# Optimization experiments

Measured on AMD Instinct MI355X. Metric: run time of the kernel, lower is better.

## Reference

```python
import jax, jax.numpy as jnp
import numpy as np

B, N, K, C = 8, 4096, 16, 64
OUT = [128, 128, 128]
BN_EPS = 1e-3


def setup_inputs() -> dict:
    key = jax.random.key(0)
    ks = jax.random.split(key, 8)
    inp = {
        "points1": jax.random.normal(ks[0], (B, 3, N), jnp.float32),
        "points2": jax.random.normal(ks[1], (B, 3, N), jnp.float32),
        "features1": jax.random.normal(ks[2], (B, C, N), jnp.float32),
        "features2": jax.random.normal(ks[3], (B, C, N), jnp.float32),
    }
    dims = [2 * C + 3] + OUT  # [131, 128, 128, 128]
    for i in range(len(OUT)):
        kw = jax.random.fold_in(ks[4], i)
        inp[f"W{i}"] = jax.random.normal(kw, (dims[i + 1], dims[i]), jnp.float32) / np.sqrt(dims[i]).astype(np.float32)
        inp[f"b{i}"] = jnp.zeros((dims[i + 1],), jnp.float32)
        inp[f"gamma{i}"] = jnp.ones((dims[i + 1],), jnp.float32)
        inp[f"beta{i}"] = jnp.zeros((dims[i + 1],), jnp.float32)
    return inp


def _knn_group(points2, points1, features2):
    # points*: [B, 3, N].  For each query in points1, find K nearest in points2.
    d = jnp.sum((points1[:, :, :, None] - points2[:, :, None, :]) ** 2, axis=1)  # [B, Nq, Ns]
    _, idx = jax.lax.top_k(-d, K)  # [B, Nq, K]
    idx_b = idx[:, None, :, :]  # [B, 1, Nq, K] broadcasts over channel dim
    xyz_g = jnp.take_along_axis(points2[:, :, None, :], idx_b, axis=3)      # [B, 3, Nq, K]
    rel_xyz = xyz_g - points1[:, :, :, None]                                # relative coords
    feat_g = jnp.take_along_axis(features2[:, :, None, :], idx_b, axis=3)  # [B, C, Nq, K]
    return jnp.concatenate([rel_xyz, feat_g], axis=1)  # [B, C+3, Nq, K]


def _conv_bn_relu(x, W, b, gamma, beta):
    # 1x1 conv == per-position channel matmul; BN in training mode (batch stats, biased var)
    x = jnp.einsum('oc,bcnk->bonk', W, x) + b[None, :, None, None]
    mu = jnp.mean(x, axis=(0, 2, 3), keepdims=True)
    var = jnp.var(x, axis=(0, 2, 3), keepdims=True)
    x = (x - mu) * jax.lax.rsqrt(var + BN_EPS)
    x = x * gamma[None, :, None, None] + beta[None, :, None, None]
    return jax.nn.relu(x)


def reference(points1, points2, features1, features2,
              W0, b0, gamma0, beta0,
              W1, b1, gamma1, beta1,
              W2, b2, gamma2, beta2):
    g = _knn_group(points2, points1, features2)                       # [B, C+3, N, K]
    f1 = jnp.broadcast_to(features1[:, :, :, None], (B, C, N, K))     # expand over neighbors
    x = jnp.concatenate([g, f1], axis=1)                              # [B, 2C+3, N, K]
    x = _conv_bn_relu(x, W0, b0, gamma0, beta0)
    x = _conv_bn_relu(x, W1, b1, gamma1, beta1)
    x = _conv_bn_relu(x, W2, b2, gamma2, beta2)
    return jnp.max(x, axis=3)                                         # [B, OUT[-1], N]
```

## Files before the change

kernel.cpp:

```cpp
#include <hip/hip_runtime.h>
#include <hip/hip_bf16.h>

#define B_ 8
#define N_ 4096
#define K_ 16
#define C_ 64
#define NK_ (N_*K_)
#define M_ (B_*N_*K_)
#define BN_EPS_ 0.001f
#define CH_ 16
#define CS_ (N_/CH_)
#define Q_ (B_*N_)
#define NB1_ (M_/128)

typedef short bf16x8 __attribute__((ext_vector_type(8)));
typedef float f32x4 __attribute__((ext_vector_type(4)));

static __device__ __forceinline__ unsigned pk2bf(float a, float b) {
  union { __hip_bfloat162 h; unsigned u; } c;
  c.h = __float22bfloat162_rn(make_float2(a, b));
  return c.u;
}
static __device__ __forceinline__ unsigned short f2bf1(float x) {
  union { __hip_bfloat16 h; unsigned short u; } c;
  c.h = __float2bfloat16(x);
  return c.u;
}

__global__ __launch_bounds__(256) void pack_pts(const float* __restrict__ p,
                                                float4* __restrict__ pf4) {
  int i = blockIdx.x * 256 + threadIdx.x;
  int b = i >> 12;
  int n = i & (N_ - 1);
  const float* base = p + (size_t)b * 3 * N_;
  pf4[i] = make_float4(base[n], base[N_ + n], base[2 * N_ + n], 0.f);
}

__global__ __launch_bounds__(256) void wcvt(const float* __restrict__ W,
                                            unsigned short* __restrict__ Wb) {
  int i = blockIdx.x * 256 + threadIdx.x;
  Wb[i] = f2bf1(W[i]);
}

__global__ void make_w0at(const float* __restrict__ W0, float* __restrict__ w0at) {
  int o = threadIdx.x;
  for (int d = 0; d < 3; ++d) w0at[d * 128 + o] = W0[o * 131 + d];
}

__global__ void zero_stats(float* __restrict__ stats) {
  int i = blockIdx.x * 256 + threadIdx.x;
  stats[i] = 0.f;
}

__global__ __launch_bounds__(64) void knn_part(const float4* __restrict__ p1f4,
                                               const float4* __restrict__ p2f4,
                                               float* __restrict__ pvals) {
  int lane = threadIdx.x;
  int blk = blockIdx.x;
  int chunk = blk & (CH_ - 1);
  int grp = (blk >> 4) & 63;
  int b = blk >> 10;
  int n1 = (grp << 6) + lane;
  int q = (b << 12) + n1;
  float4 qv = p1f4[q];
  float ax = qv.x, ay = qv.y, az = qv.z;
  const float4* pb = p2f4 + ((size_t)b << 12) + chunk * CS_;

  float s[16];
  #pragma unroll
  for (int i = 0; i < 16; ++i) s[i] = 3.0e38f;

  #pragma unroll 8
  for (int t = 0; t < CS_; ++t) {
    float4 c = pb[t];
    float dx = ax - c.x, dy = ay - c.y, dz = az - c.z;
    float d = __fadd_rn(__fadd_rn(__fmul_rn(dx, dx), __fmul_rn(dy, dy)), __fmul_rn(dz, dz));
    #pragma unroll
    for (int i = 0; i < 15; ++i) s[i] = __builtin_amdgcn_fmed3f(s[i], s[i + 1], d);
    s[15] = fminf(s[15], d);
  }
  #pragma unroll
  for (int i = 0; i < 16; ++i) pvals[(size_t)(chunk * 16 + i) * Q_ + q] = s[i];
}

__global__ __launch_bounds__(256) void knn_merge(const float* __restrict__ pvals,
                                                 float* __restrict__ Tarr) {
  int q = blockIdx.x * 256 + threadIdx.x;
  float s[16];
  #pragma unroll
  for (int i = 0; i < 16; ++i) s[i] = 3.0e38f;
  #pragma unroll 8
  for (int t = 0; t < CH_ * 16; ++t) {
    float d = pvals[(size_t)t * Q_ + q];
    #pragma unroll
    for (int i = 0; i < 15; ++i) s[i] = __builtin_amdgcn_fmed3f(s[i], s[i + 1], d);
    s[15] = fminf(s[15], d);
  }
  Tarr[q] = s[0];
}

__global__ __launch_bounds__(64) void knn_cand(const float4* __restrict__ p1f4,
                                               const float4* __restrict__ p2f4,
                                               const float* __restrict__ Tarr,
                                               int* __restrict__ cidx,
                                               int* __restrict__ ccnt) {
  int lane = threadIdx.x;
  int blk = blockIdx.x;
  int chunk = blk & (CH_ - 1);
  int grp = (blk >> 4) & 63;
  int b = blk >> 10;
  int n1 = (grp << 6) + lane;
  int q = (b << 12) + n1;
  float4 qq = p1f4[q];
  float ax = qq.x, ay = qq.y, az = qq.z;
  const float4* pb = p2f4 + ((size_t)b << 12) + chunk * CS_;
  float T = Tarr[q];
  int cnt = 0;
  int base = (q * CH_ + chunk) * 16;
  #pragma unroll 4
  for (int t = 0; t < CS_; ++t) {
    float4 c = pb[t];
    float dx = ax - c.x, dy = ay - c.y, dz = az - c.z;
    float d = __fadd_rn(__fadd_rn(__fmul_rn(dx, dx), __fmul_rn(dy, dy)), __fmul_rn(dz, dz));
    if (d <= T && cnt < 16) { cidx[base + cnt] = chunk * CS_ + t; ++cnt; }
  }
  ccnt[q * CH_ + chunk] = cnt;
}

__global__ __launch_bounds__(256) void knn_combine(const int* __restrict__ cidx,
                                                   const int* __restrict__ ccnt,
                                                   int* __restrict__ idxout) {
  int q = blockIdx.x * 256 + threadIdx.x;
  int tot = 0;
  int ob = q * 16;
  for (int c = 0; c < CH_; ++c) {
    int m = ccnt[q * CH_ + c];
    const int* src = cidx + (size_t)(q * CH_ + c) * 16;
    for (int i = 0; i < m && tot < 16; ++i) idxout[ob + tot++] = src[i];
  }
}

__global__ __launch_bounds__(256) void pkern(const float* __restrict__ f,
                                             const float* __restrict__ W0,
                                             const float* __restrict__ bias,
                                             const float4* __restrict__ pf4,
                                             const float* __restrict__ w0at,
                                             float sgn,
                                             float* __restrict__ P, int coff) {
  __shared__ float fx[32 * 65];
  __shared__ __align__(16) float Wl[64 * 132];
  int tid = threadIdx.x;
  int bn0 = blockIdx.x * 32;
  int b = bn0 >> 12, nb0 = bn0 & (N_ - 1);

  for (int u = tid; u < 32 * 64; u += 256) {
    int c = u >> 5, nl = u & 31;
    fx[nl * 65 + c] = f[((size_t)b * C_ + c) * N_ + nb0 + nl];
  }
  for (int u = tid; u < 128 * 64; u += 256) {
    int o = u >> 6, c = u & 63;
    Wl[c * 132 + o] = W0[o * 131 + coff + c];
  }
  __syncthreads();

  int og = tid & 15, np_ = tid >> 4;
  int o0 = og * 8;
  int na = np_ * 2, nb = na + 1;
  float acc0[8], acc1[8];
  #pragma unroll
  for (int j = 0; j < 8; ++j) {
    float bv = bias ? bias[o0 + j] : 0.f;
    acc0[j] = bv; acc1[j] = bv;
  }
  for (int c = 0; c < 64; ++c) {
    float x0 = fx[na * 65 + c], x1 = fx[nb * 65 + c];
    float4 wa = *(const float4*)&Wl[c * 132 + o0];
    float4 wb = *(const float4*)&Wl[c * 132 + o0 + 4];
    float w[8] = {wa.x, wa.y, wa.z, wa.w, wb.x, wb.y, wb.z, wb.w};
    #pragma unroll
    for (int j = 0; j < 8; ++j) {
      acc0[j] = fmaf(x0, w[j], acc0[j]);
      acc1[j] = fmaf(x1, w[j], acc1[j]);
    }
  }
  float4 pa = pf4[bn0 + na], pb_ = pf4[bn0 + nb];
  #pragma unroll
  for (int j = 0; j < 8; ++j) {
    float wx = w0at[o0 + j], wy = w0at[128 + o0 + j], wz = w0at[256 + o0 + j];
    acc0[j] += sgn * (wx * pa.x + wy * pa.y + wz * pa.z);
    acc1[j] += sgn * (wx * pb_.x + wy * pb_.y + wz * pb_.z);
  }
  float* Pa = P + (size_t)(bn0 + na) * 128 + o0;
  float* Pb = P + (size_t)(bn0 + nb) * 128 + o0;
  *(float4*)Pa = make_float4(acc0[0], acc0[1], acc0[2], acc0[3]);
  *(float4*)(Pa + 4) = make_float4(acc0[4], acc0[5], acc0[6], acc0[7]);
  *(float4*)Pb = make_float4(acc1[0], acc1[1], acc1[2], acc1[3]);
  *(float4*)(Pb + 4) = make_float4(acc1[4], acc1[5], acc1[6], acc1[7]);
}

__global__ __launch_bounds__(256) void gstats_kernel(
    const float* __restrict__ A, const float* __restrict__ Bv,
    const int* __restrict__ idx, unsigned short* __restrict__ x0b,
    float* __restrict__ part) {
  __shared__ float sred[4 * 128 * 2];
  int tid = threadIdx.x;
  int R0 = blockIdx.x * 128;
  int b = R0 >> 16;
  int n0 = (R0 & (NK_ - 1)) >> 4;
  int cc = (tid & 15) * 8;
  int r0l = tid >> 4;

  int jj[8];
  #pragma unroll
  for (int p = 0; p < 8; ++p) jj[p] = idx[R0 + r0l + p * 16];

  float ssum[8], ssq[8];
  #pragma unroll
  for (int u = 0; u < 8; ++u) { ssum[u] = 0.f; ssq[u] = 0.f; }

  #pragma unroll
  for (int p = 0; p < 8; ++p) {
    const float* Ar = A + (size_t)((b << 12) + n0 + p) * 128 + cc;
    const float* Br = Bv + (size_t)((b << 12) + jj[p]) * 128 + cc;
    float av[8], bv[8];
    *(float4*)&av[0] = *(const float4*)Ar;  *(float4*)&av[4] = *(const float4*)(Ar + 4);
    *(float4*)&bv[0] = *(const float4*)Br;  *(float4*)&bv[4] = *(const float4*)(Br + 4);
    unsigned pw[4];
    #pragma unroll
    for (int i = 0; i < 4; ++i)
      pw[i] = pk2bf(av[2 * i] + bv[2 * i], av[2 * i + 1] + bv[2 * i + 1]);
    uint4 pk; pk.x = pw[0]; pk.y = pw[1]; pk.z = pw[2]; pk.w = pw[3];
    *(uint4*)(x0b + (size_t)(R0 + r0l + p * 16) * 128 + cc) = pk;
    #pragma unroll
    for (int i = 0; i < 4; ++i) {
      float q0 = __uint_as_float(pw[i] << 16);
      float q1 = __uint_as_float(pw[i] & 0xFFFF0000u);
      ssum[2 * i] += q0;     ssq[2 * i] = fmaf(q0, q0, ssq[2 * i]);
      ssum[2 * i + 1] += q1; ssq[2 * i + 1] = fmaf(q1, q1, ssq[2 * i + 1]);
    }
  }
  int w = tid >> 6, lane = tid & 63;
  #pragma unroll
  for (int u = 0; u < 8; ++u) {
    ssum[u] += __shfl_xor(ssum[u], 16);
    ssum[u] += __shfl_xor(ssum[u], 32);
    ssq[u] += __shfl_xor(ssq[u], 16);
    ssq[u] += __shfl_xor(ssq[u], 32);
  }
  if (lane < 16) {
    #pragma unroll
    for (int u = 0; u < 8; ++u) {
      sred[(w * 128 + lane * 8 + u) * 2] = ssum[u];
      sred[(w * 128 + lane * 8 + u) * 2 + 1] = ssq[u];
    }
  }
  __syncthreads();
  if (tid < 128) {
    float a = 0.f, q2 = 0.f;
    #pragma unroll
    for (int ww = 0; ww < 4; ++ww) {
      a += sred[(ww * 128 + tid) * 2];
      q2 += sred[(ww * 128 + tid) * 2 + 1];
    }
    part[(size_t)blockIdx.x * 256 + tid] = a;
    part[(size_t)blockIdx.x * 256 + 128 + tid] = q2;
  }
}

__global__ __launch_bounds__(256) void reduce_atomic(const float* __restrict__ part,
                                                     float* __restrict__ statso) {
  int tid = threadIdx.x;
  int r0 = blockIdx.x * 16;
  float a = 0.f;
  #pragma unroll
  for (int i = 0; i < 16; ++i) a += part[(size_t)(r0 + i) * 256 + tid];
  atomicAdd(statso + tid, a);
}

__global__ void bnfin_kernel(const float* __restrict__ stats, const float* __restrict__ gamma,
                             const float* __restrict__ beta, float* __restrict__ bnp) {
  int o = threadIdx.x;
  const float invM = 1.0f / (float)M_;
  float mean = stats[o] * invM;
  float var = stats[128 + o] * invM - mean * mean;
  float s = gamma[o] * rsqrtf(var + BN_EPS_);
  bnp[o] = s;
  bnp[128 + o] = beta[o] - mean * s;
}

static __device__ __forceinline__ char* xsa(unsigned short* Xs, int row, int bytecol) {
  return (char*)Xs + row * 256 + (bytecol ^ ((row & 7) << 4));
}

static __device__ __forceinline__ void stage_lin(
    unsigned short* Xs, const unsigned short* x0b, const float* bnp0,
    int R0, int tid) {
  int cc = (tid & 15) * 8;
  int r0l = tid >> 4;
  float svv[8], tvv[8];
  *(float4*)&svv[0] = *(const float4*)(bnp0 + cc);       *(float4*)&svv[4] = *(const float4*)(bnp0 + cc + 4);
  *(float4*)&tvv[0] = *(const float4*)(bnp0 + 128 + cc); *(float4*)&tvv[4] = *(const float4*)(bnp0 + 132 + cc);
  #pragma unroll
  for (int p = 0; p < 8; ++p) {
    uint4 pv = *(const uint4*)(x0b + (size_t)(R0 + r0l + p * 16) * 128 + cc);
    float xv[8];
    xv[0] = __uint_as_float(pv.x << 16); xv[1] = __uint_as_float(pv.x & 0xFFFF0000u);
    xv[2] = __uint_as_float(pv.y << 16); xv[3] = __uint_as_float(pv.y & 0xFFFF0000u);
    xv[4] = __uint_as_float(pv.z << 16); xv[5] = __uint_as_float(pv.z & 0xFFFF0000u);
    xv[6] = __uint_as_float(pv.w << 16); xv[7] = __uint_as_float(pv.w & 0xFFFF0000u);
    float y[8];
    #pragma unroll
    for (int u = 0; u < 8; ++u) y[u] = fmaxf(fmaf(svv[u], xv[u], tvv[u]), 0.f);
    uint4 pk;
    pk.x = pk2bf(y[0], y[1]); pk.y = pk2bf(y[2], y[3]);
    pk.z = pk2bf(y[4], y[5]); pk.w = pk2bf(y[6], y[7]);
    *(uint4*)xsa(Xs, r0l + p * 16, 16 * (tid & 15)) = pk;
  }
}

__global__ __launch_bounds__(256) void pass1_kernel(
    const unsigned short* __restrict__ x0b, const float* __restrict__ bnp0,
    const unsigned short* __restrict__ W1b, const float* __restrict__ b1,
    float* __restrict__ part) {
  __shared__ __align__(16) unsigned short Xs[128 * 128];
  int tid = threadIdx.x;
  int R0 = blockIdx.x * 128;

  stage_lin(Xs, x0b, bnp0, R0, tid);

  int w = tid >> 6, lane = tid & 63;
  int m16 = lane & 15, qd = lane >> 4;

  bf16x8 bf[2][4];
  #pragma unroll
  for (int nt = 0; nt < 2; ++nt) {
    const unsigned short* wb = W1b + (size_t)(w * 32 + nt * 16 + m16) * 128 + qd * 8;
    #pragma unroll
    for (int q = 0; q < 4; ++q) bf[nt][q] = *(const bf16x8*)(wb + q * 32);
  }
  __syncthreads();

  f32x4 acc[8][2];
  #pragma unroll
  for (int m = 0; m < 8; ++m) {
    acc[m][0] = (f32x4){0.f, 0.f, 0.f, 0.f};
    acc[m][1] = (f32x4){0.f, 0.f, 0.f, 0.f};
  }
  #pragma unroll
  for (int m = 0; m < 8; ++m) {
    bf16x8 a[4];
    #pragma unroll
    for (int q = 0; q < 4; ++q) a[q] = *(const bf16x8*)xsa(Xs, m * 16 + m16, 16 * qd + 64 * q);
    #pragma unroll
    for (int q = 0; q < 4; ++q) {
      acc[m][0] = __builtin_amdgcn_mfma_f32_16x16x32_bf16(a[q], bf[0][q], acc[m][0], 0, 0, 0);
      acc[m][1] = __builtin_amdgcn_mfma_f32_16x16x32_bf16(a[q], bf[1][q], acc[m][1], 0, 0, 0);
    }
  }

  float ssum[2] = {0.f, 0.f}, ssq[2] = {0.f, 0.f};
  #pragma unroll
  for (int nt = 0; nt < 2; ++nt) {
    float bb = b1[w * 32 + nt * 16 + m16];
    #pragma unroll
    for (int m = 0; m < 8; ++m)
      #pragma unroll
      for (int rg = 0; rg < 4; ++rg) {
        float y = acc[m][nt][rg] + bb;
        ssum[nt] += y;
        ssq[nt] = fmaf(y, y, ssq[nt]);
      }
  }
  #pragma unroll
  for (int nt = 0; nt < 2; ++nt) {
    ssum[nt] += __shfl_xor(ssum[nt], 16);
    ssum[nt] += __shfl_xor(ssum[nt], 32);
    ssq[nt] += __shfl_xor(ssq[nt], 16);
    ssq[nt] += __shfl_xor(ssq[nt], 32);
  }
  if (lane < 16) {
    size_t pb = (size_t)blockIdx.x * 256 + w * 32;
    #pragma unroll
    for (int nt = 0; nt < 2; ++nt) {
      part[pb + nt * 16 + lane] = ssum[nt];
      part[pb + 128 + nt * 16 + lane] = ssq[nt];
    }
  }
}

__global__ __launch_bounds__(256) void pass2_kernel(
    const unsigned short* __restrict__ x0b, const float* __restrict__ bnp0,
    const unsigned short* __restrict__ W1b, const float* __restrict__ b1,
    const float* __restrict__ bnp1, const unsigned short* __restrict__ W2b,
    const float* __restrict__ b2, float* __restrict__ ymaxo,
    float* __restrict__ ymino, float* __restrict__ part) {
  __shared__ __align__(16) unsigned short Xs[128 * 128];
  int tid = threadIdx.x;
  int R0 = blockIdx.x * 128;
  int b = R0 >> 16;
  int n0 = (R0 & (NK_ - 1)) >> 4;

  stage_lin(Xs, x0b, bnp0, R0, tid);

  int w = tid >> 6, lane = tid & 63;
  int m16 = lane & 15, qd = lane >> 4;

  bf16x8 bf[2][4];
  #pragma unroll
  for (int nt = 0; nt < 2; ++nt) {
    const unsigned short* wb = W1b + (size_t)(w * 32 + nt * 16 + m16) * 128 + qd * 8;
    #pragma unroll
    for (int q = 0; q < 4; ++q) bf[nt][q] = *(const bf16x8*)(wb + q * 32);
  }
  __syncthreads();

  f32x4 acc[8][2];
  #pragma unroll
  for (int m = 0; m < 8; ++m) {
    acc[m][0] = (f32x4){0.f, 0.f, 0.f, 0.f};
    acc[m][1] = (f32x4){0.f, 0.f, 0.f, 0.f};
  }
  #pragma unroll
  for (int m = 0; m < 8; ++m) {
    bf16x8 a[4];
    #pragma unroll
    for (int q = 0; q < 4; ++q) a[q] = *(const bf16x8*)xsa(Xs, m * 16 + m16, 16 * qd + 64 * q);
    #pragma unroll
    for (int q = 0; q < 4; ++q) {
      acc[m][0] = __builtin_amdgcn_mfma_f32_16x16x32_bf16(a[q], bf[0][q], acc[m][0], 0, 0, 0);
      acc[m][1] = __builtin_amdgcn_mfma_f32_16x16x32_bf16(a[q], bf[1][q], acc[m][1], 0, 0, 0);
    }
  }
  __syncthreads();

  #pragma unroll
  for (int nt = 0; nt < 2; ++nt) {
    int col = w * 32 + nt * 16 + m16;
    float sc = bnp1[col];
    float tc = fmaf(sc, b1[col], bnp1[128 + col]);
    #pragma unroll
    for (int m = 0; m < 8; ++m)
      #pragma unroll
      for (int rg = 0; rg < 4; ++rg) {
        int row = m * 16 + qd * 4 + rg;
        float y = fmaxf(fmaf(sc, acc[m][nt][rg], tc), 0.f);
        *(unsigned short*)xsa(Xs, row, 2 * col) = f2bf1(y);
      }
  }

  bf16x8 bf2[2][4];
  #pragma unroll
  for (int nt = 0; nt < 2; ++nt) {
    const unsigned short* wb = W2b + (size_t)(w * 32 + nt * 16 + m16) * 128 + qd * 8;
    #pragma unroll
    for (int q = 0; q < 4; ++q) bf2[nt][q] = *(const bf16x8*)(wb + q * 32);
  }
  __syncthreads();

  #pragma unroll
  for (int m = 0; m < 8; ++m) {
    acc[m][0] = (f32x4){0.f, 0.f, 0.f, 0.f};
    acc[m][1] = (f32x4){0.f, 0.f, 0.f, 0.f};
  }
  #pragma unroll
  for (int m = 0; m < 8; ++m) {
    bf16x8 a[4];
    #pragma unroll
    for (int q = 0; q < 4; ++q) a[q] = *(const bf16x8*)xsa(Xs, m * 16 + m16, 16 * qd + 64 * q);
    #pragma unroll
    for (int q = 0; q < 4; ++q) {
      acc[m][0] = __builtin_amdgcn_mfma_f32_16x16x32_bf16(a[q], bf2[0][q], acc[m][0], 0, 0, 0);
      acc[m][1] = __builtin_amdgcn_mfma_f32_16x16x32_bf16(a[q], bf2[1][q], acc[m][1], 0, 0, 0);
    }
  }

  float ssum[2] = {0.f, 0.f}, ssq[2] = {0.f, 0.f};
  #pragma unroll
  for (int nt = 0; nt < 2; ++nt) {
    float bb = b2[w * 32 + nt * 16 + m16];
    #pragma unroll
    for (int m = 0; m < 8; ++m) {
      float y0 = acc[m][nt][0] + bb;
      float mx = y0, mn = y0, su = y0, sq = y0 * y0;
      #pragma unroll
      for (int rg = 1; rg < 4; ++rg) {
        float y = acc[m][nt][rg] + bb;
        mx = fmaxf(mx, y); mn = fminf(mn, y);
        su += y; sq = fmaf(y, y, sq);
      }
      mx = fmaxf(mx, __shfl_xor(mx, 16)); mx = fmaxf(mx, __shfl_xor(mx, 32));
      mn = fminf(mn, __shfl_xor(mn, 16)); mn = fminf(mn, __shfl_xor(mn, 32));
      ssum[nt] += su; ssq[nt] += sq;
      if (lane < 16) {
        int n = n0 + m;
        size_t basey = ((size_t)(b << 12) + n) * 128 + w * 32 + nt * 16 + lane;
        ymaxo[basey] = mx;
        ymino[basey] = mn;
      }
    }
  }
  #pragma unroll
  for (int nt = 0; nt < 2; ++nt) {
    ssum[nt] += __shfl_xor(ssum[nt], 16);
    ssum[nt] += __shfl_xor(ssum[nt], 32);
    ssq[nt] += __shfl_xor(ssq[nt], 16);
    ssq[nt] += __shfl_xor(ssq[nt], 32);
  }
  if (lane < 16) {
    size_t pb = (size_t)blockIdx.x * 256 + w * 32;
    #pragma unroll
    for (int nt = 0; nt < 2; ++nt) {
      part[pb + nt * 16 + lane] = ssum[nt];
      part[pb + 128 + nt * 16 + lane] = ssq[nt];
    }
  }
}

__global__ __launch_bounds__(256) void final_kernel(const float* __restrict__ ymaxo,
                                                    const float* __restrict__ ymino,
                                                    const float* __restrict__ bnp2,
                                                    float* __restrict__ out) {
  __shared__ float T[64 * 129];
  int tid = threadIdx.x;
  int b = blockIdx.x >> 6;
  int n0 = (blockIdx.x & 63) * 64;
  for (int u = tid; u < 64 * 128; u += 256) {
    int nl = u >> 7, o = u & 127;
    size_t base = ((size_t)(b << 12) + n0 + nl) * 128 + o;
    float s = bnp2[o], t = bnp2[128 + o];
    float v = fmaf(s, (s >= 0.f ? ymaxo[base] : ymino[base]), t);
    T[nl * 129 + o] = fmaxf(v, 0.f);
  }
  __syncthreads();
  for (int u = tid; u < 64 * 128; u += 256) {
    int o = u >> 6, nl = u & 63;
    out[((size_t)b * 128 + o) * N_ + n0 + nl] = T[nl * 129 + o];
  }
}

extern "C" void kernel_launch(void* const* d_in, const int* in_sizes, int n_in,
                              void* d_out, int out_size, void* d_ws, size_t ws_size,
                              hipStream_t stream) {
  (void)in_sizes; (void)n_in; (void)out_size; (void)ws_size;
  const float* points1 = (const float*)d_in[0];
  const float* points2 = (const float*)d_in[1];
  const float* features1 = (const float*)d_in[2];
  const float* features2 = (const float*)d_in[3];
  const float* W0 = (const float*)d_in[4];
  const float* b0 = (const float*)d_in[5];
  const float* g0 = (const float*)d_in[6];
  const float* be0 = (const float*)d_in[7];
  const float* W1 = (const float*)d_in[8];
  const float* b1 = (const float*)d_in[9];
  const float* g1 = (const float*)d_in[10];
  const float* be1 = (const float*)d_in[11];
  const float* W2 = (const float*)d_in[12];
  const float* b2 = (const float*)d_in[13];
  const float* g2 = (const float*)d_in[14];
  const float* be2 = (const float*)d_in[15];
  float* out = (float*)d_out;

  char* ws = (char*)d_ws;
  size_t off = 0;
  auto alloc = [&](size_t bytes) -> void* {
    void* p = ws + off;
    off += (bytes + 255) & ~(size_t)255;
    return p;
  };
  int* idx = (int*)alloc((size_t)M_ * 4);
  float4* p1f4 = (float4*)alloc((size_t)B_ * N_ * 16);
  float4* p2f4 = (float4*)alloc((size_t)B_ * N_ * 16);
  float* A = (float*)alloc((size_t)B_ * N_ * 128 * 4);
  float* Bv = (float*)alloc((size_t)B_ * N_ * 128 * 4);
  unsigned short* W1b = (unsigned short*)alloc(128 * 128 * 2);
  unsigned short* W2b = (unsigned short*)alloc(128 * 128 * 2);
  float* w0at = (float*)alloc(3 * 128 * 4);
  float* stats = (float*)alloc(3 * 256 * 4);
  float* bnp = (float*)alloc(3 * 256 * 4);
  float* ymaxo = (float*)alloc((size_t)B_ * N_ * 128 * 4);
  float* ymino = (float*)alloc((size_t)B_ * N_ * 128 * 4);
  char* bigbuf = (char*)alloc((size_t)128 * 1024 * 1024);
  float* pvals = (float*)bigbuf;
  int* cidx = (int*)(bigbuf + (size_t)32 * 1024 * 1024);
  int* ccnt = (int*)(bigbuf + (size_t)64 * 1024 * 1024);
  float* Tarr = (float*)(bigbuf + (size_t)66 * 1024 * 1024);
  unsigned short* x0b = (unsigned short*)bigbuf;

  float* part0 = ymaxo;
  float* part1 = ymino;
  float* part2 = A;

  zero_stats<<<3, 256, 0, stream>>>(stats);
  pack_pts<<<B_ * N_ / 256, 256, 0, stream>>>(points1, p1f4);
  pack_pts<<<B_ * N_ / 256, 256, 0, stream>>>(points2, p2f4);
  wcvt<<<64, 256, 0, stream>>>(W1, W1b);
  wcvt<<<64, 256, 0, stream>>>(W2, W2b);
  make_w0at<<<1, 128, 0, stream>>>(W0, w0at);

  knn_part<<<B_ * 64 * CH_, 64, 0, stream>>>(p1f4, p2f4, pvals);
  knn_merge<<<Q_ / 256, 256, 0, stream>>>(pvals, Tarr);
  knn_cand<<<B_ * 64 * CH_, 64, 0, stream>>>(p1f4, p2f4, Tarr, cidx, ccnt);
  knn_combine<<<Q_ / 256, 256, 0, stream>>>(cidx, ccnt, idx);

  pkern<<<B_ * N_ / 32, 256, 0, stream>>>(features1, W0, b0, p1f4, w0at, -1.f, A, 67);
  pkern<<<B_ * N_ / 32, 256, 0, stream>>>(features2, W0, nullptr, p2f4, w0at, 1.f, Bv, 3);

  gstats_kernel<<<NB1_, 256, 0, stream>>>(A, Bv, idx, x0b, part0);
  reduce_atomic<<<NB1_ / 16, 256, 0, stream>>>(part0, stats);
  bnfin_kernel<<<1, 128, 0, stream>>>(stats, g0, be0, bnp);

  pass1_kernel<<<NB1_, 256, 0, stream>>>(x0b, bnp, W1b, b1, part1);
  reduce_atomic<<<NB1_ / 16, 256, 0, stream>>>(part1, stats + 256);
  bnfin_kernel<<<1, 128, 0, stream>>>(stats + 256, g1, be1, bnp + 256);

  pass2_kernel<<<NB1_, 256, 0, stream>>>(x0b, bnp, W1b, b1, bnp + 256,
                                         W2b, b2, ymaxo, ymino, part2);
  reduce_atomic<<<NB1_ / 16, 256, 0, stream>>>(part2, stats + 512);
  bnfin_kernel<<<1, 128, 0, stream>>>(stats + 512, g2, be2, bnp + 512);

  final_kernel<<<B_ * N_ / 64, 256, 0, stream>>>(ymaxo, ymino, bnp + 512, out);
}
```

Baseline: 495.3 us.

## Derive KNN threshold from a point subset, then filter and select candidates

New measurement: 624.7 us. 26.1% more time.

```diff
diff --git a/kernel.cpp b/kernel.cpp
--- a/kernel.cpp
+++ b/kernel.cpp
@@ -8,10 +8,9 @@
 #define NK_ (N_*K_)
 #define M_ (B_*N_*K_)
 #define BN_EPS_ 0.001f
-#define CH_ 16
-#define CS_ (N_/CH_)
 #define Q_ (B_*N_)
 #define NB1_ (M_/128)
+#define CAP_ 48
 
 typedef short bf16x8 __attribute__((ext_vector_type(8)));
 typedef float f32x4 __attribute__((ext_vector_type(4)));
@@ -25,6 +24,11 @@
   union { __hip_bfloat16 h; unsigned short u; } c;
   c.h = __float2bfloat16(x);
   return c.u;
+}
+
+static __device__ __forceinline__ float knn_key(float ax, float ay, float az, float4 c) {
+  float dx = ax - c.x, dy = ay - c.y, dz = az - c.z;
+  return __fadd_rn(__fadd_rn(__fmul_rn(dx, dx), __fmul_rn(dy, dy)), __fmul_rn(dz, dz));
 }
 
 __global__ __launch_bounds__(256) void pack_pts(const float* __restrict__ p,
@@ -52,45 +56,42 @@
   stats[i] = 0.f;
 }
 
-__global__ __launch_bounds__(64) void knn_part(const float4* __restrict__ p1f4,
-                                               const float4* __restrict__ p2f4,
-                                               float* __restrict__ pvals) {
+__global__ __launch_bounds__(64) void knn_sub(const float4* __restrict__ p1f4,
+                                              const float4* __restrict__ p2f4,
+                                              float* __restrict__ pvals) {
   int lane = threadIdx.x;
   int blk = blockIdx.x;
-  int chunk = blk & (CH_ - 1);
-  int grp = (blk >> 4) & 63;
-  int b = blk >> 10;
-  int n1 = (grp << 6) + lane;
-  int q = (b << 12) + n1;
+  int c = blk & 3;
+  int grp = (blk >> 2) & 63;
+  int b = blk >> 8;
+  int q = (b << 12) + (grp << 6) + lane;
   float4 qv = p1f4[q];
   float ax = qv.x, ay = qv.y, az = qv.z;
-  const float4* pb = p2f4 + ((size_t)b << 12) + chunk * CS_;
+  const float4* pb = p2f4 + ((size_t)b << 12) + c * 128;
 
   float s[16];
   #pragma unroll
   for (int i = 0; i < 16; ++i) s[i] = 3.0e38f;
 
   #pragma unroll 8
-  for (int t = 0; t < CS_; ++t) {
-    float4 c = pb[t];
-    float dx = ax - c.x, dy = ay - c.y, dz = az - c.z;
-    float d = __fadd_rn(__fadd_rn(__fmul_rn(dx, dx), __fmul_rn(dy, dy)), __fmul_rn(dz, dz));
+  for (int t = 0; t < 128; ++t) {
+    float d = knn_key(ax, ay, az, pb[t]);
     #pragma unroll
     for (int i = 0; i < 15; ++i) s[i] = __builtin_amdgcn_fmed3f(s[i], s[i + 1], d);
     s[15] = fminf(s[15], d);
   }
   #pragma unroll
-  for (int i = 0; i < 16; ++i) pvals[(size_t)(chunk * 16 + i) * Q_ + q] = s[i];
-}
-
-__global__ __launch_bounds__(256) void knn_merge(const float* __restrict__ pvals,
-                                                 float* __restrict__ Tarr) {
+  for (int i = 0; i < 16; ++i) pvals[(size_t)(c * 16 + i) * Q_ + q] = s[i];
+}
+
+__global__ __launch_bounds__(256) void knn_t0(const float* __restrict__ pvals,
+                                              float* __restrict__ Tarr) {
   int q = blockIdx.x * 256 + threadIdx.x;
   float s[16];
   #pragma unroll
   for (int i = 0; i < 16; ++i) s[i] = 3.0e38f;
   #pragma unroll 8
-  for (int t = 0; t < CH_ * 16; ++t) {
+  for (int t = 0; t < 64; ++t) {
     float d = pvals[(size_t)t * Q_ + q];
     #pragma unroll
     for (int i = 0; i < 15; ++i) s[i] = __builtin_amdgcn_fmed3f(s[i], s[i + 1], d);
@@ -99,44 +100,61 @@
   Tarr[q] = s[0];
 }
 
-__global__ __launch_bounds__(64) void knn_cand(const float4* __restrict__ p1f4,
-                                               const float4* __restrict__ p2f4,
-                                               const float* __restrict__ Tarr,
-                                               int* __restrict__ cidx,
-                                               int* __restrict__ ccnt) {
+__global__ __launch_bounds__(64) void knn_collect(const float4* __restrict__ p1f4,
+                                                  const float4* __restrict__ p2f4,
+                                                  const float* __restrict__ Tarr,
+                                                  uint2* __restrict__ cbuf,
+                                                  int* __restrict__ ccnt) {
   int lane = threadIdx.x;
   int blk = blockIdx.x;
-  int chunk = blk & (CH_ - 1);
-  int grp = (blk >> 4) & 63;
-  int b = blk >> 10;
-  int n1 = (grp << 6) + lane;
-  int q = (b << 12) + n1;
-  float4 qq = p1f4[q];
-  float ax = qq.x, ay = qq.y, az = qq.z;
-  const float4* pb = p2f4 + ((size_t)b << 12) + chunk * CS_;
+  int c = blk & 7;
+  int grp = (blk >> 3) & 63;
+  int b = blk >> 9;
+  int q = (b << 12) + (grp << 6) + lane;
+  float4 qv = p1f4[q];
+  float ax = qv.x, ay = qv.y, az = qv.z;
+  const float4* pb = p2f4 + ((size_t)b << 12) + c * 512;
   float T = Tarr[q];
   int cnt = 0;
-  int base = (q * CH_ + chunk) * 16;
   #pragma unroll 4
-  for (int t = 0; t < CS_; ++t) {
-    float4 c = pb[t];
-    float dx = ax - c.x, dy = ay - c.y, dz = az - c.z;
-    float d = __fadd_rn(__fadd_rn(__fmul_rn(dx, dx), __fmul_rn(dy, dy)), __fmul_rn(dz, dz));
-    if (d <= T && cnt < 16) { cidx[base + cnt] = chunk * CS_ + t; ++cnt; }
-  }
-  ccnt[q * CH_ + chunk] = cnt;
-}
-
-__global__ __launch_bounds__(256) void knn_combine(const int* __restrict__ cidx,
-                                                   const int* __restrict__ ccnt,
-                                                   int* __restrict__ idxout) {
+  for (int t = 0; t < 512; ++t) {
+    float d = knn_key(ax, ay, az, pb[t]);
+    if (d <= T && cnt < CAP_) {
+      cbuf[(size_t)(c * CAP_ + cnt) * Q_ + q] = make_uint2(__float_as_uint(d), c * 512 + t);
+      ++cnt;
+    }
+  }
+  ccnt[c * Q_ + q] = cnt;
+}
+
+__global__ __launch_bounds__(256) void knn_final(const uint2* __restrict__ cbuf,
+                                                 const int* __restrict__ ccnt,
+                                                 int* __restrict__ idxout) {
   int q = blockIdx.x * 256 + threadIdx.x;
-  int tot = 0;
-  int ob = q * 16;
-  for (int c = 0; c < CH_; ++c) {
-    int m = ccnt[q * CH_ + c];
-    const int* src = cidx + (size_t)(q * CH_ + c) * 16;
-    for (int i = 0; i < m && tot < 16; ++i) idxout[ob + tot++] = src[i];
+  float s[16];
+  #pragma unroll
+  for (int i = 0; i < 16; ++i) s[i] = 3.0e38f;
+  int cn[8];
+  #pragma unroll
+  for (int c = 0; c < 8; ++c) {
+    int m = ccnt[c * Q_ + q];
+    cn[c] = m;
+    for (int i = 0; i < m; ++i) {
+      float d = __uint_as_float(cbuf[(size_t)(c * CAP_ + i) * Q_ + q].x);
+      #pragma unroll
+      for (int k = 0; k < 15; ++k) s[k] = __builtin_amdgcn_fmed3f(s[k], s[k + 1], d);
+      s[15] = fminf(s[15], d);
+    }
+  }
+  float T = s[0];
+  int tot = 0, ob = q * 16;
+  #pragma unroll
+  for (int c = 0; c < 8; ++c) {
+    int m = cn[c];
+    for (int i = 0; i < m && tot < 16; ++i) {
+      uint2 e = cbuf[(size_t)(c * CAP_ + i) * Q_ + q];
+      if (__uint_as_float(e.x) <= T) idxout[ob + tot++] = (int)e.y;
+    }
   }
 }
 
@@ -580,10 +598,10 @@
   float* ymaxo = (float*)alloc((size_t)B_ * N_ * 128 * 4);
   float* ymino = (float*)alloc((size_t)B_ * N_ * 128 * 4);
   char* bigbuf = (char*)alloc((size_t)128 * 1024 * 1024);
-  float* pvals = (float*)bigbuf;
-  int* cidx = (int*)(bigbuf + (size_t)32 * 1024 * 1024);
-  int* ccnt = (int*)(bigbuf + (size_t)64 * 1024 * 1024);
-  float* Tarr = (float*)(bigbuf + (size_t)66 * 1024 * 1024);
+  uint2* cbuf = (uint2*)bigbuf;
+  float* pvals = (float*)(bigbuf + (size_t)98 * 1024 * 1024);
+  float* Tarr = (float*)(bigbuf + (size_t)107 * 1024 * 1024);
+  int* ccnt = (int*)(bigbuf + (size_t)108 * 1024 * 1024);
   unsigned short* x0b = (unsigned short*)bigbuf;
 
   float* part0 = ymaxo;
@@ -597,10 +615,10 @@
   wcvt<<<64, 256, 0, stream>>>(W2, W2b);
   make_w0at<<<1, 128, 0, stream>>>(W0, w0at);
 
-  knn_part<<<B_ * 64 * CH_, 64, 0, stream>>>(p1f4, p2f4, pvals);
-  knn_merge<<<Q_ / 256, 256, 0, stream>>>(pvals, Tarr);
-  knn_cand<<<B_ * 64 * CH_, 64, 0, stream>>>(p1f4, p2f4, Tarr, cidx, ccnt);
-  knn_combine<<<Q_ / 256, 256, 0, stream>>>(cidx, ccnt, idx);
+  knn_sub<<<B_ * 64 * 4, 64, 0, stream>>>(p1f4, p2f4, pvals);
+  knn_t0<<<Q_ / 256, 256, 0, stream>>>(pvals, Tarr);
+  knn_collect<<<B_ * 64 * 8, 64, 0, stream>>>(p1f4, p2f4, Tarr, cbuf, ccnt);
+  knn_final<<<Q_ / 256, 256, 0, stream>>>(cbuf, ccnt, idx);
 
   pkern<<<B_ * N_ / 32, 256, 0, stream>>>(features1, W0, b0, p1f4, w0at, -1.f, A, 67);
   pkern<<<B_ * N_ / 32, 256, 0, stream>>>(features2, W0, nullptr, p2f4, w0at, 1.f, Bv, 3);
```
